# Performance work log

Measured on AMD Instinct MI355X. Metric: run time of the kernel, lower is better.

The kernel has to match this reference:

```python
import jax, jax.numpy as jnp
import numpy as np

N_AREA = 10000
N_FEAT = 16
HID = 64
N_EDGE = 320000
BATCH = 64
EPS = 1e-5
SLOPE = 0.01  # F.leaky_relu default negative_slope


def _layer_norm(x, g, b):
    mu = jnp.mean(x, axis=-1, keepdims=True)
    var = jnp.mean(jnp.square(x - mu), axis=-1, keepdims=True)
    return (x - mu) * jax.lax.rsqrt(var + EPS) * g + b


def _leaky(x):
    return jnp.where(x >= 0, x, SLOPE * x)


def setup_inputs() -> dict:
    key = jax.random.key(0)
    ks = jax.random.split(key, 8)
    inp = {}
    inp["state"] = jax.random.normal(ks[0], (BATCH, N_AREA * N_FEAT), dtype=jnp.float32)
    inp["edge_index"] = jax.random.randint(ks[1], (2, N_EDGE), 0, N_AREA, dtype=jnp.int32)
    inp["batch_size"] = BATCH
    inp["rej_rate"] = jnp.zeros((1,), jnp.float32)
    inp["theta_value"] = jnp.zeros((1,), jnp.float32)
    inp["W1"] = jax.random.normal(ks[2], (N_FEAT, HID), jnp.float32) * 0.1
    inp["b1"] = jnp.zeros((HID,), jnp.float32)
    inp["W2"] = jax.random.normal(ks[3], (HID, HID), jnp.float32) * 0.1
    inp["b2"] = jnp.zeros((HID,), jnp.float32)
    inp["W3"] = jax.random.normal(ks[4], (HID, HID), jnp.float32) * 0.1
    inp["b3"] = jnp.zeros((HID,), jnp.float32)
    inp["g1"] = jnp.ones((HID,), jnp.float32)
    inp["be1"] = jnp.zeros((HID,), jnp.float32)
    inp["g3"] = jnp.ones((HID,), jnp.float32)
    inp["be3"] = jnp.zeros((HID,), jnp.float32)
    inp["Wf"] = jax.random.normal(ks[5], (HID, HID), jnp.float32) * 0.1
    inp["bf"] = jnp.zeros((HID,), jnp.float32)
    return inp


def reference(state, edge_index, batch_size, rej_rate, theta_value,
              W1, b1, W2, b2, W3, b3, g1, be1, g3, be3, Wf, bf):
    B = batch_size
    x = state.reshape(B, N_AREA, N_FEAT)
    # GCN normalization with self-loops (PyG GCNConv default)
    loops = jnp.arange(N_AREA, dtype=edge_index.dtype)
    src = jnp.concatenate([edge_index[0], loops])
    dst = jnp.concatenate([edge_index[1], loops])
    deg = jnp.zeros((N_AREA,), state.dtype).at[dst].add(1.0)
    dinv = jax.lax.rsqrt(jnp.maximum(deg, 1.0))  # deg >= 1 due to self-loops
    norm = dinv[src] * dinv[dst]  # [E+N]

    def conv(h, W, b):
        hw = h @ W                                  # [B, N, H]
        msg = hw[:, src, :] * norm[None, :, None]   # gather over sources
        out = jnp.zeros((B, N_AREA, W.shape[1]), hw.dtype).at[:, dst, :].add(msg)
        return out + b

    h1 = _leaky(_layer_norm(conv(x, W1, b1), g1, be1))
    h2 = _leaky(conv(h1, W2, b2)) + h1
    h3 = _leaky(_layer_norm(conv(h2, W3, b3), g3, be3)) + h1
    out = jnp.tanh(h3 @ Wf + bf)
    return out.reshape(B, -1)
```

## Files before the change

### kernel.cpp

```cpp
#include <hip/hip_runtime.h>
#include <hip/hip_fp16.h>
#include <cstdint>
#include <cstddef>

#define N_AREA 10000
#define N_FEAT 16
#define HID 64
#define BATCH 64
#define EPSL 1e-5f
#define SLOPE 0.01f
#define NCHUNK 157

typedef float fv4 __attribute__((ext_vector_type(4)));
typedef _Float16 h4 __attribute__((ext_vector_type(4)));

__device__ __forceinline__ float lrelu(float x) { return x >= 0.f ? x : SLOPE * x; }
__device__ __forceinline__ float tanh_fast(float x) {
    float t = __expf(2.0f * x);
    return 1.0f - 2.0f / (t + 1.0f);
}
__device__ __forceinline__ float2 h2f2(unsigned u) {
    return __half22float2(*reinterpret_cast<const __half2*>(&u));
}
__device__ __forceinline__ unsigned f2h2(float a, float b) {
    __half2 h = __floats2half2_rn(a, b);
    return *reinterpret_cast<const unsigned*>(&h);
}
__device__ __forceinline__ h4 pack4(float a, float b, float c, float d) {
    auto p0 = __builtin_amdgcn_cvt_pkrtz(a, b);
    auto p1 = __builtin_amdgcn_cvt_pkrtz(c, d);
    h4 r;
    *reinterpret_cast<decltype(p0)*>(&r) = p0;
    *(reinterpret_cast<decltype(p0)*>(&r) + 1) = p1;
    return r;
}

__global__ __launch_bounds__(256) void k_zero(int* p, int n) {
    int i = blockIdx.x * 256 + threadIdx.x;
    if (i < n) p[i] = 0;
}

__global__ __launch_bounds__(256) void k_hist(const int* __restrict__ dst, int* __restrict__ counts, int E) {
    int e = blockIdx.x * 256 + threadIdx.x;
    if (e < E) atomicAdd(&counts[dst[e]], 1);
}

__global__ __launch_bounds__(256) void k_wcvt(const float* __restrict__ Wa, const float* __restrict__ Wb,
                                              const float* __restrict__ Wc, _Float16* __restrict__ fa,
                                              _Float16* __restrict__ fb, _Float16* __restrict__ fc) {
    int t = threadIdx.x;
    int lane = t & 63, pg = t >> 6;
    int g = lane >> 4, q = lane & 15;
    for (int p = pg; p < 16; p += 4) {
        int mt = p >> 2, kk = p & 3;
        int sb = (16 * kk + 4 * g) * HID + 16 * mt + q;
        int dst = (p * 64 + lane) * 4;
        for (int i = 0; i < 4; ++i) {
            fa[dst + i] = (_Float16)Wa[sb + i * HID];
            fb[dst + i] = (_Float16)Wb[sb + i * HID];
            fc[dst + i] = (_Float16)Wc[sb + i * HID];
        }
    }
}

__global__ __launch_bounds__(1024) void k_scan(const int* __restrict__ counts, int* __restrict__ offsets,
                                               int* __restrict__ cursor, float* __restrict__ dinv,
                                               int2* __restrict__ ew) {
    const int PER = 10;
    int t = threadIdx.x;
    int base = t * PER;
    int local[PER];
    int sum = 0;
#pragma unroll
    for (int i = 0; i < PER; ++i) {
        int idx = base + i;
        int c = (idx < N_AREA) ? (((counts[idx] + 1) + 3) & ~3) : 0;
        local[i] = sum;
        sum += c;
    }
    __shared__ int part[1024];
    part[t] = sum;
    __syncthreads();
    for (int off = 1; off < 1024; off <<= 1) {
        int v = (t >= off) ? part[t - off] : 0;
        __syncthreads();
        part[t] += v;
        __syncthreads();
    }
    int excl = (t == 0) ? 0 : part[t - 1];
    if (t == 1023) {
        int tot = part[1023];
        offsets[N_AREA] = tot;
        for (int i = 0; i < 64; ++i) ew[tot + i] = make_int2(0, 0);
    }
    for (int i = 0; i < PER; ++i) {
        int idx = base + i;
        if (idx < N_AREA) {
            int off = excl + local[i];
            offsets[idx] = off;
            int c = counts[idx] + 1;
            int pc = (c + 3) & ~3;
            float dv = rsqrtf((float)c);
            dinv[idx] = dv;
            ew[off] = make_int2(idx, __float_as_int(dv * dv));
            for (int pp = c; pp < pc; ++pp) ew[off + pp] = make_int2(idx, 0);
            cursor[idx] = off + 1;
        }
    }
}

__global__ __launch_bounds__(256) void k_scatter(const int* __restrict__ ei, const float* __restrict__ dinv,
                                                 int* __restrict__ cursor, int2* __restrict__ ew, int E) {
    int e = blockIdx.x * 256 + threadIdx.x;
    if (e < E) {
        int s = ei[e], d = ei[E + e];
        int p = atomicAdd(&cursor[d], 1);
        ew[p] = make_int2(s, __float_as_int(dinv[s] * dinv[d]));
    }
}

__global__ __launch_bounds__(256, 8) void k_conv1(const float* __restrict__ state, const float* __restrict__ W1,
                                                  const float* __restrict__ b1, const float* __restrict__ g1,
                                                  const float* __restrict__ be1, unsigned short* __restrict__ h1,
                                                  const int* __restrict__ offs, const int2* __restrict__ ew) {
    __shared__ float xs[64][20];
    __shared__ float ws[16][64];
    int blk = blockIdx.x;
    int xc = blk & 7, ii = blk >> 3;
    int b = xc + 8 * (ii / NCHUNK);
    int c = ii % NCHUNK;
    int n0 = c * 64;
    int t = threadIdx.x;
    *(float4*)&ws[t >> 4][(t & 15) * 4] = *(const float4*)(W1 + (t >> 4) * HID + (t & 15) * 4);
    int ln = t >> 2, q = t & 3;
    int n = n0 + ln;
    const float* sb = state + (size_t)b * (N_AREA * N_FEAT);
    float4 acc = make_float4(0.f, 0.f, 0.f, 0.f);
    if (n < N_AREA) {
        int beg = offs[n], end = offs[n + 1];
        for (int e = beg; e < end; ++e) {
            int2 sw = ew[e];
            float w = __int_as_float(sw.y);
            float4 v = *(const float4*)(sb + (size_t)sw.x * N_FEAT + q * 4);
            acc.x += w * v.x; acc.y += w * v.y; acc.z += w * v.z; acc.w += w * v.w;
        }
    }
    *(float4*)&xs[ln][q * 4] = acc;
    __syncthreads();
    int wave = t >> 6, lane = t & 63;
    float bias = b1[lane], gg = g1[lane], bb = be1[lane];
    for (int j = 0; j < 16; ++j) {
        int lnn = wave * 16 + j;
        float a = bias;
#pragma unroll
        for (int f = 0; f < N_FEAT; ++f) a += xs[lnn][f] * ws[f][lane];
        float s = a;
#pragma unroll
        for (int m = 1; m < 64; m <<= 1) s += __shfl_xor(s, m);
        float mu = s * (1.0f / 64.0f);
        float dv = a - mu;
        float qv = dv * dv;
#pragma unroll
        for (int m = 1; m < 64; m <<= 1) qv += __shfl_xor(qv, m);
        float rstd = rsqrtf(qv * (1.0f / 64.0f) + EPSL);
        float y = lrelu(dv * rstd * gg + bb);
        int nn = n0 + lnn;
        unsigned hv = (unsigned)__half_as_ushort(__float2half_rn(y));
        unsigned ov = (unsigned)__shfl_xor((int)hv, 1);
        if (((lane & 1) == 0) && nn < N_AREA)
            *(unsigned*)(h1 + (size_t)b * (N_AREA * HID) + (size_t)nn * HID + lane) = hv | (ov << 16);
    }
}

template <int EPI>
__global__ __launch_bounds__(256, 8) void k_conv(const unsigned short* __restrict__ src,
                                                 const _Float16* __restrict__ Wfrag,
                                                 const float* __restrict__ bias, const float* __restrict__ g,
                                                 const float* __restrict__ be, const unsigned short* __restrict__ resid,
                                                 void* __restrict__ out, const int* __restrict__ offs,
                                                 const int2* __restrict__ ew, const _Float16* __restrict__ WfFrag,
                                                 const float* __restrict__ bf) {
    __shared__ float a_t[64][68];
    __shared__ int2 echunk[4][64];
    int blk = blockIdx.x;
    int xc = blk & 7, ii = blk >> 3;
    int b = xc + 8 * (ii / NCHUNK);
    int c = ii % NCHUNK;
    int n0 = c * 64;
    int t = threadIdx.x;
    int lane = t & 63;
    int wave = __builtin_amdgcn_readfirstlane(t) >> 6;
    int q = lane >> 4;
    int ql = lane & 15;
    int f4 = ql * 4;
    const unsigned short* sp = src + (size_t)b * (N_AREA * HID);
    const _Float16* spH = (const _Float16*)sp;
    int nb = n0 + wave * 16;
    int beg = 0, end = 0;
    if (nb < N_AREA) { beg = offs[nb]; end = offs[nb + 1]; }
    int2 eC = ew[beg + lane];
    for (int j = 0; j < 16; ++j) {
        int n = nb + j;
        int cnt = (n < N_AREA) ? (end - beg) : 0;
        int nbeg = end;
        int nend = (n + 1 < N_AREA) ? offs[n + 2] : end;
        int2 eN = ew[nbeg + lane];
        echunk[wave][lane] = eC;
        int cmin = cnt > 64 ? 64 : cnt;
        fv4 a0 = {0.f, 0.f, 0.f, 0.f}, a1 = a0, a2 = a0, a3 = a0;
        int k16 = cmin >> 4;
        for (int k = 0; k < k16; ++k) {
            int e0 = 16 * k + 4 * q;
            int2 ea = echunk[wave][e0 + 0];
            int2 eb = echunk[wave][e0 + 1];
            int2 ec = echunk[wave][e0 + 2];
            int2 ed = echunk[wave][e0 + 3];
            h4 va = *(const h4*)(spH + (unsigned)ea.x * HID + f4);
            h4 vb = *(const h4*)(spH + (unsigned)eb.x * HID + f4);
            h4 vc = *(const h4*)(spH + (unsigned)ec.x * HID + f4);
            h4 vd = *(const h4*)(spH + (unsigned)ed.x * HID + f4);
            float wa = __int_as_float(ea.y), wb = __int_as_float(eb.y);
            float wc = __int_as_float(ec.y), wd = __int_as_float(ed.y);
            a0.x += wa * (float)va[0]; a0.y += wa * (float)va[1]; a0.z += wa * (float)va[2]; a0.w += wa * (float)va[3];
            a1.x += wb * (float)vb[0]; a1.y += wb * (float)vb[1]; a1.z += wb * (float)vb[2]; a1.w += wb * (float)vb[3];
            a2.x += wc * (float)vc[0]; a2.y += wc * (float)vc[1]; a2.z += wc * (float)vc[2]; a2.w += wc * (float)vc[3];
            a3.x += wd * (float)vd[0]; a3.y += wd * (float)vd[1]; a3.z += wd * (float)vd[2]; a3.w += wd * (float)vd[3];
        }
        for (int e4 = k16 * 16; e4 < cmin; e4 += 4) {
            int2 ea = echunk[wave][e4 + q];
            h4 va = *(const h4*)(spH + (unsigned)ea.x * HID + f4);
            float wa = __int_as_float(ea.y);
            a0.x += wa * (float)va[0]; a0.y += wa * (float)va[1]; a0.z += wa * (float)va[2]; a0.w += wa * (float)va[3];
        }
        if (cnt > 64) {
            for (int e = beg + 64; e < end; e += 4) {
                int2 ea = ew[e + q];
                h4 va = *(const h4*)(spH + (unsigned)ea.x * HID + f4);
                float wa = __int_as_float(ea.y);
                a0.x += wa * (float)va[0]; a0.y += wa * (float)va[1]; a0.z += wa * (float)va[2]; a0.w += wa * (float)va[3];
            }
        }
        fv4 acc = (a0 + a1) + (a2 + a3);
        acc.x += __shfl_xor(acc.x, 16); acc.y += __shfl_xor(acc.y, 16);
        acc.z += __shfl_xor(acc.z, 16); acc.w += __shfl_xor(acc.w, 16);
        acc.x += __shfl_xor(acc.x, 32); acc.y += __shfl_xor(acc.y, 32);
        acc.z += __shfl_xor(acc.z, 32); acc.w += __shfl_xor(acc.w, 32);
        if (q == 0) {
            int ln = wave * 16 + j;
            int colp = 4 * ((ln >> 2) ^ (ql & 7)) + (ln & 3);
            a_t[f4 + 0][colp] = acc.x;
            a_t[f4 + 1][colp] = acc.y;
            a_t[f4 + 2][colp] = acc.z;
            a_t[f4 + 3][colp] = acc.w;
        }
        eC = eN; beg = nbeg; end = nend;
    }
    __syncthreads();
    fv4 acc[4] = {{0.f, 0.f, 0.f, 0.f}, {0.f, 0.f, 0.f, 0.f}, {0.f, 0.f, 0.f, 0.f}, {0.f, 0.f, 0.f, 0.f}};
#pragma unroll
    for (int kk = 0; kk < 4; ++kk) {
        int f0 = 16 * kk + 4 * q;
        int colp = 4 * ((4 * wave + (ql >> 2)) ^ ((4 * kk + q) & 7)) + (ql & 3);
        float b0 = a_t[f0 + 0][colp];
        float b1 = a_t[f0 + 1][colp];
        float b2 = a_t[f0 + 2][colp];
        float b3 = a_t[f0 + 3][colp];
        h4 bfr = pack4(b0, b1, b2, b3);
#pragma unroll
        for (int mt = 0; mt < 4; ++mt) {
            h4 af = *(const h4*)(Wfrag + ((mt * 4 + kk) * 64 + lane) * 4);
            acc[mt] = __builtin_amdgcn_mfma_f32_16x16x16f16(af, bfr, acc[mt], 0, 0, 0);
        }
    }
    int nd = n0 + 16 * wave + ql;
#pragma unroll
    for (int mt = 0; mt < 4; ++mt) {
        float4 bv = *(const float4*)(bias + 16 * mt + 4 * q);
        acc[mt].x += bv.x; acc[mt].y += bv.y; acc[mt].z += bv.z; acc[mt].w += bv.w;
    }
    if constexpr (EPI >= 1) {
        float s = 0.f, qv = 0.f;
#pragma unroll
        for (int mt = 0; mt < 4; ++mt) {
            s += acc[mt].x + acc[mt].y + acc[mt].z + acc[mt].w;
            qv += acc[mt].x * acc[mt].x + acc[mt].y * acc[mt].y + acc[mt].z * acc[mt].z + acc[mt].w * acc[mt].w;
        }
        s += __shfl_xor(s, 16); s += __shfl_xor(s, 32);
        qv += __shfl_xor(qv, 16); qv += __shfl_xor(qv, 32);
        float mu = s * (1.0f / 64.0f);
        float var = qv * (1.0f / 64.0f) - mu * mu;
        float rstd = rsqrtf(var + EPSL);
#pragma unroll
        for (int mt = 0; mt < 4; ++mt) {
            float4 gv = *(const float4*)(g + 16 * mt + 4 * q);
            float4 bev = *(const float4*)(be + 16 * mt + 4 * q);
            acc[mt].x = (acc[mt].x - mu) * rstd * gv.x + bev.x;
            acc[mt].y = (acc[mt].y - mu) * rstd * gv.y + bev.y;
            acc[mt].z = (acc[mt].z - mu) * rstd * gv.z + bev.z;
            acc[mt].w = (acc[mt].w - mu) * rstd * gv.w + bev.w;
        }
    }
    const unsigned short* rb = resid + (size_t)b * (N_AREA * HID);
    if constexpr (EPI == 0) {
        unsigned short* ob = (unsigned short*)out + (size_t)b * (N_AREA * HID);
        if (nd < N_AREA) {
            size_t rowo = (size_t)nd * HID;
#pragma unroll
            for (int mt = 0; mt < 4; ++mt) {
                int fo = 16 * mt + 4 * q;
                uint2 rr = *(const uint2*)(rb + rowo + fo);
                float2 r01 = h2f2(rr.x), r23 = h2f2(rr.y);
                float o0 = lrelu(acc[mt].x) + r01.x;
                float o1 = lrelu(acc[mt].y) + r01.y;
                float o2 = lrelu(acc[mt].z) + r23.x;
                float o3 = lrelu(acc[mt].w) + r23.y;
                uint2 st;
                st.x = f2h2(o0, o1);
                st.y = f2h2(o2, o3);
                *(uint2*)(ob + rowo + fo) = st;
            }
        }
    } else {
        int ncl = nd < N_AREA ? nd : (N_AREA - 1);
        size_t rowo = (size_t)ncl * HID;
        h4 h3f[4];
#pragma unroll
        for (int mt = 0; mt < 4; ++mt) {
            int fo = 16 * mt + 4 * q;
            uint2 rr = *(const uint2*)(rb + rowo + fo);
            float2 r01 = h2f2(rr.x), r23 = h2f2(rr.y);
            float v0 = lrelu(acc[mt].x) + r01.x;
            float v1 = lrelu(acc[mt].y) + r01.y;
            float v2 = lrelu(acc[mt].z) + r23.x;
            float v3 = lrelu(acc[mt].w) + r23.y;
            h3f[mt] = pack4(v0, v1, v2, v3);
        }
        fv4 acc2[4] = {{0.f, 0.f, 0.f, 0.f}, {0.f, 0.f, 0.f, 0.f}, {0.f, 0.f, 0.f, 0.f}, {0.f, 0.f, 0.f, 0.f}};
#pragma unroll
        for (int kk = 0; kk < 4; ++kk) {
#pragma unroll
            for (int mt = 0; mt < 4; ++mt) {
                h4 af = *(const h4*)(WfFrag + ((mt * 4 + kk) * 64 + lane) * 4);
                acc2[mt] = __builtin_amdgcn_mfma_f32_16x16x16f16(af, h3f[kk], acc2[mt], 0, 0, 0);
            }
        }
        float* ob = (float*)out + (size_t)b * (N_AREA * HID);
        if (nd < N_AREA) {
#pragma unroll
            for (int mt = 0; mt < 4; ++mt) {
                float4 bfv = *(const float4*)(bf + 16 * mt + 4 * q);
                float4 o;
                o.x = tanh_fast(acc2[mt].x + bfv.x);
                o.y = tanh_fast(acc2[mt].y + bfv.y);
                o.z = tanh_fast(acc2[mt].z + bfv.z);
                o.w = tanh_fast(acc2[mt].w + bfv.w);
                *(float4*)(ob + (size_t)nd * HID + 16 * mt + 4 * q) = o;
            }
        }
    }
}

extern "C" void kernel_launch(void* const* d_in, const int* in_sizes, int n_in,
                              void* d_out, int out_size, void* d_ws, size_t ws_size,
                              hipStream_t stream) {
    const float* state = (const float*)d_in[0];
    const int* ei = (const int*)d_in[1];
    const int E = in_sizes[1] / 2;
    const float* W1 = (const float*)d_in[5];
    const float* b1 = (const float*)d_in[6];
    const float* W2 = (const float*)d_in[7];
    const float* b2 = (const float*)d_in[8];
    const float* W3 = (const float*)d_in[9];
    const float* b3 = (const float*)d_in[10];
    const float* g1 = (const float*)d_in[11];
    const float* be1 = (const float*)d_in[12];
    const float* g3 = (const float*)d_in[13];
    const float* be3 = (const float*)d_in[14];
    const float* Wf = (const float*)d_in[15];
    const float* bf = (const float*)d_in[16];
    float* out = (float*)d_out;

    uint8_t* base = (uint8_t*)d_ws;
    size_t off = 0;
    auto carve = [&](size_t bytes) {
        void* p = base + off;
        off = (off + bytes + 255) & ~(size_t)255;
        return p;
    };
    float* dinv = (float*)carve(N_AREA * 4);
    int* counts = (int*)carve(N_AREA * 4);
    int* offsets = (int*)carve((N_AREA + 1) * 4);
    int* cursor = (int*)carve(N_AREA * 4);
    int2* ew = (int2*)carve(((size_t)E + 4 * N_AREA + 64) * 8);
    unsigned short* h1 = (unsigned short*)carve((size_t)BATCH * N_AREA * HID * 2);
    unsigned short* h2 = (unsigned short*)carve((size_t)BATCH * N_AREA * HID * 2);
    _Float16* w2f = (_Float16*)carve(4096 * 2);
    _Float16* w3f = (_Float16*)carve(4096 * 2);
    _Float16* wff = (_Float16*)carve(4096 * 2);

    const int GRID = 8 * NCHUNK * (BATCH / 8);

    k_zero<<<(N_AREA + 255) / 256, 256, 0, stream>>>(counts, N_AREA);
    k_hist<<<(E + 255) / 256, 256, 0, stream>>>(ei + E, counts, E);
    k_wcvt<<<1, 256, 0, stream>>>(W2, W3, Wf, w2f, w3f, wff);
    k_scan<<<1, 1024, 0, stream>>>(counts, offsets, cursor, dinv, ew);
    k_scatter<<<(E + 255) / 256, 256, 0, stream>>>(ei, dinv, cursor, ew, E);

    k_conv1<<<GRID, 256, 0, stream>>>(state, W1, b1, g1, be1, h1, offsets, ew);
    k_conv<0><<<GRID, 256, 0, stream>>>(h1, w2f, b2, nullptr, nullptr, h1, h2, offsets, ew, nullptr, nullptr);
    k_conv<2><<<GRID, 256, 0, stream>>>(h2, w3f, b3, g3, be3, h1, out, offsets, ew, wff, bf);
}
```

Baseline: 1.041 ms.

## Restructure conv1 gather to wave-per-node with LDS-staged edge chunks

The first-layer aggregation changes from four threads per node walking edges serially to one wavefront per node. Each wave prefetches 64 edge records into shared memory, 8 edges are processed in parallel per step with 8 lanes each loading float2 feature pairs, and the partial sums are reduced with cross-lane shuffles. Per-node edge lists are now padded to multiples of 8 instead of 4, and the edge buffer is enlarged to match. The goal is more memory-level parallelism and coalesced edge loads for the gather. The cost is extra padding work, shuffle reductions, and serialization over 16 nodes per wave.

```diff
diff --git a/kernel.cpp b/kernel.cpp
--- a/kernel.cpp
+++ b/kernel.cpp
@@ -74,7 +74,7 @@
 #pragma unroll
     for (int i = 0; i < PER; ++i) {
         int idx = base + i;
-        int c = (idx < N_AREA) ? (((counts[idx] + 1) + 3) & ~3) : 0;
+        int c = (idx < N_AREA) ? (((counts[idx] + 1) + 7) & ~7) : 0;
         local[i] = sum;
         sum += c;
     }
@@ -99,7 +99,7 @@
             int off = excl + local[i];
             offsets[idx] = off;
             int c = counts[idx] + 1;
-            int pc = (c + 3) & ~3;
+            int pc = (c + 7) & ~7;
             float dv = rsqrtf((float)c);
             dinv[idx] = dv;
             ew[off] = make_int2(idx, __float_as_int(dv * dv));
@@ -125,6 +125,7 @@
                                                   const int* __restrict__ offs, const int2* __restrict__ ew) {
     __shared__ float xs[64][20];
     __shared__ float ws[16][64];
+    __shared__ int2 echunk1[4][64];
     int blk = blockIdx.x;
     int xc = blk & 7, ii = blk >> 3;
     int b = xc + 8 * (ii / NCHUNK);
@@ -132,22 +133,60 @@
     int n0 = c * 64;
     int t = threadIdx.x;
     *(float4*)&ws[t >> 4][(t & 15) * 4] = *(const float4*)(W1 + (t >> 4) * HID + (t & 15) * 4);
-    int ln = t >> 2, q = t & 3;
-    int n = n0 + ln;
-    const float* sb = state + (size_t)b * (N_AREA * N_FEAT);
-    float4 acc = make_float4(0.f, 0.f, 0.f, 0.f);
-    if (n < N_AREA) {
-        int beg = offs[n], end = offs[n + 1];
-        for (int e = beg; e < end; ++e) {
-            int2 sw = ew[e];
-            float w = __int_as_float(sw.y);
-            float4 v = *(const float4*)(sb + (size_t)sw.x * N_FEAT + q * 4);
-            acc.x += w * v.x; acc.y += w * v.y; acc.z += w * v.z; acc.w += w * v.w;
-        }
-    }
-    *(float4*)&xs[ln][q * 4] = acc;
+    int lane = t & 63;
+    int wave = __builtin_amdgcn_readfirstlane(t) >> 6;
+    int q8 = lane >> 3;
+    int f2 = lane & 7;
+    const float2* s2 = (const float2*)(state + (size_t)b * (N_AREA * N_FEAT));
+    int nb = n0 + wave * 16;
+    int beg = 0, end = 0;
+    if (nb < N_AREA) { beg = offs[nb]; end = offs[nb + 1]; }
+    int2 eC = ew[beg + lane];
+    for (int j = 0; j < 16; ++j) {
+        int n = nb + j;
+        int cnt = (n < N_AREA) ? (end - beg) : 0;
+        int nbeg = end;
+        int nend = (n + 1 < N_AREA) ? offs[n + 2] : end;
+        int2 eN = ew[nbeg + lane];
+        echunk1[wave][lane] = eC;
+        int cmin = cnt > 64 ? 64 : cnt;
+        float2 a0 = make_float2(0.f, 0.f), a1 = a0;
+        int k16 = cmin >> 4;
+        for (int k = 0; k < k16; ++k) {
+            int2 ea = echunk1[wave][16 * k + q8];
+            int2 eb = echunk1[wave][16 * k + 8 + q8];
+            float2 va = s2[(unsigned)ea.x * 8 + f2];
+            float2 vb = s2[(unsigned)eb.x * 8 + f2];
+            float wa = __int_as_float(ea.y), wb = __int_as_float(eb.y);
+            a0.x += wa * va.x; a0.y += wa * va.y;
+            a1.x += wb * vb.x; a1.y += wb * vb.y;
+        }
+        for (int e8 = k16 * 16; e8 < cmin; e8 += 8) {
+            int2 ea = echunk1[wave][e8 + q8];
+            float2 va = s2[(unsigned)ea.x * 8 + f2];
+            float wa = __int_as_float(ea.y);
+            a0.x += wa * va.x; a0.y += wa * va.y;
+        }
+        if (cnt > 64) {
+            for (int e = beg + 64; e < end; e += 8) {
+                int2 ea = ew[e + q8];
+                float2 va = s2[(unsigned)ea.x * 8 + f2];
+                float wa = __int_as_float(ea.y);
+                a0.x += wa * va.x; a0.y += wa * va.y;
+            }
+        }
+        float2 acc = make_float2(a0.x + a1.x, a0.y + a1.y);
+        acc.x += __shfl_xor(acc.x, 8);  acc.y += __shfl_xor(acc.y, 8);
+        acc.x += __shfl_xor(acc.x, 16); acc.y += __shfl_xor(acc.y, 16);
+        acc.x += __shfl_xor(acc.x, 32); acc.y += __shfl_xor(acc.y, 32);
+        if (q8 == 0) {
+            int ln = wave * 16 + j;
+            xs[ln][f2 * 2 + 0] = acc.x;
+            xs[ln][f2 * 2 + 1] = acc.y;
+        }
+        eC = eN; beg = nbeg; end = nend;
+    }
     __syncthreads();
-    int wave = t >> 6, lane = t & 63;
     float bias = b1[lane], gg = g1[lane], bb = be1[lane];
     for (int j = 0; j < 16; ++j) {
         int lnn = wave * 16 + j;
@@ -391,7 +430,7 @@
     int* counts = (int*)carve(N_AREA * 4);
     int* offsets = (int*)carve((N_AREA + 1) * 4);
     int* cursor = (int*)carve(N_AREA * 4);
-    int2* ew = (int2*)carve(((size_t)E + 4 * N_AREA + 64) * 8);
+    int2* ew = (int2*)carve(((size_t)E + 8 * N_AREA + 64) * 8);
     unsigned short* h1 = (unsigned short*)carve((size_t)BATCH * N_AREA * HID * 2);
     unsigned short* h2 = (unsigned short*)carve((size_t)BATCH * N_AREA * HID * 2);
     _Float16* w2f = (_Float16*)carve(4096 * 2);
```

New measurement: 1.012 ms. 2.8% less time.
